# Performance work log

Hardware: AMD Instinct MI355X
Metric: run time of the kernel (lower is better)

## Reference

```python
import jax, jax.numpy as jnp
import numpy as np

B, T, C, D = 4, 2048, 48, 512
L = 16                    # transcript length per video (distinct labels)
K = 9                     # bdy_kernel
CS = 15                   # cs_kernel
N_TR = L - 1
N_CAND = 3 * N_TR         # candidate_mul * pt_num
WIN_LEN = int(T / L * 0.15)   # int(t / t_len * win_scale)
ALPHA, BETA, GAMMA, TEMP = 1.0, 1.0, 0.1, 0.1
LOG2 = float(np.log(2.0))

def _bdy_kernel():
    ker = np.zeros((K, K), np.float32)
    c = K // 2
    ker[:c, :c] = 1; ker[c:, c:] = 1
    ker[:c, c:] = -1; ker[c:, :c] = -1
    ker[c, c] = 0
    return jnp.asarray(ker)

BDY_KER = _bdy_kernel()

def bdy_score_fn(prob):
    # prob: [T, C]; sliding windows of size K over time (zero padded)
    c = K // 2
    pad = jnp.pad(prob, ((c, c), (0, 0)))
    win = pad[jnp.arange(T)[:, None] + jnp.arange(K)[None, :]]       # [T,K,C]
    p = win[:, :, None, :]                                           # [T,K,1,C]
    m = (p + win[:, None, :, :]) / 2                                 # [T,K,K,C]
    # torch F.kl_div((m+1e-32).log(), p) = p*(log p - log(m+1e-32)), xlogy(0)=0
    kl = jnp.sum(jnp.where(p > 0, p * (jnp.log(jnp.where(p > 0, p, 1.0)) - jnp.log(m + 1e-32)), 0.0), -1)
    js = (kl + jnp.swapaxes(kl, 1, 2)) / 2
    js = -(js / LOG2 * 2 - 1)                                        # [T,K,K]
    return jnp.mean(BDY_KER[None] * js, axis=(-1, -2))               # [T]

def dp(cls_score):
    # cls_score: [N_TR, N_CAND]; min-cost alignment DP, inner jj-loop vectorized
    cost = -cls_score
    n_tr, n_x = N_TR, N_CAND
    W = 2 * n_tr + 1
    col = jnp.arange(W)
    inf = jnp.float32(jnp.inf)
    tr_at = jnp.clip(col // 2, 0, n_tr - 1)
    even = (col % 2 == 0)
    ge2 = col >= 2

    def init_cols(ii):
        c0 = jnp.where(ii < n_x - n_tr, 0.0, inf)
        c1 = jnp.where(ii <= n_x - n_tr, cost[0, ii], inf)
        d1 = jnp.where(ii <= n_x - n_tr, 1, 0).astype(jnp.int32)
        return c0, c1, d1

    c0, c1, d1 = init_cols(0)
    row0 = jnp.full((W,), inf).at[0].set(c0).at[1].set(c1)
    dir0 = jnp.zeros((W,), jnp.int32).at[1].set(d1)

    def step(prev, ii):
        dm1 = jnp.concatenate([jnp.full((1,), inf), prev[:-1]])
        dm2 = jnp.concatenate([jnp.full((2,), inf), prev[:-2]])
        c_at = cost[:, ii][tr_at]
        even_val = jnp.minimum(prev, dm1)
        even_dir = jnp.where(prev < dm1, 0, 1).astype(jnp.int32)
        odd_val = c_at + jnp.minimum(dm1, dm2)
        odd_dir = jnp.where(dm1 < dm2, 1, 2).astype(jnp.int32)
        c0, c1, d1 = init_cols(ii)
        new = jnp.where(ge2, jnp.where(even, even_val, odd_val), inf)
        new = new.at[0].set(c0).at[1].set(c1)
        dirs = jnp.where(ge2, jnp.where(even, even_dir, odd_dir), 0).astype(jnp.int32)
        dirs = dirs.at[1].set(d1)
        return new, dirs

    last, dirs = jax.lax.scan(step, row0, jnp.arange(1, n_x))
    dir_mat = jnp.concatenate([dir0[None], dirs], 0)                 # [n_x, W]
    cur_j0 = jnp.where(last[2 * n_tr] < last[2 * n_tr - 1], 2 * n_tr, 2 * n_tr - 1).astype(jnp.int32)

    def bt(cur_j, x):
        ii, dir_row = x
        is_odd = (cur_j % 2) == 1
        out_idx = jnp.where(is_odd, cur_j // 2, jnp.int32(n_tr))     # n_tr = OOB -> dropped
        new_j = cur_j - dir_row[cur_j]
        return new_j, (out_idx, ii.astype(jnp.int32))

    _, (oi, ovals) = jax.lax.scan(bt, cur_j0, (jnp.arange(n_x), dir_mat), reverse=True)
    return jnp.zeros((n_tr,), jnp.int32).at[oi].set(ovals, mode='drop')

def detect(logit, tr):
    # logit: [T,C] (detached), tr: [L] ints -> boundary frame indices [N_TR]
    prob = jax.nn.softmax(logit, -1)
    score = bdy_score_fn(prob).at[0].set(-jnp.inf)
    backup = score
    pos = jnp.arange(T)

    def pick(s, _):
        i = jnp.argmax(s)
        return jnp.where(jnp.abs(pos - i) <= WIN_LEN, -jnp.inf, s), i

    _, cand = jax.lax.scan(pick, score, None, length=N_CAND)
    cand = jnp.sort(cand)                                            # [N_CAND]
    # class-transition score at candidate points
    cc = CS // 2
    pairs = jnp.pad(prob[:, tr], ((cc, cc), (0, 0)))                 # [T+2cc, L]
    win = pairs[cand[:, None] + jnp.arange(CS)[None, :]]             # [N_CAND, CS, L]
    first, second = win[:, :, :-1], win[:, :, 1:]
    k0 = jnp.where(jnp.arange(CS) < cc, 1.0, -1.0)[None, :, None]
    cls = jnp.sum(k0 * (first - second), axis=1) / (2 * CS)          # [N_CAND, N_TR]
    cls = cls.T + backup[cand][None, :]                              # [N_TR, N_CAND]
    return cand[dp(cls)]

def _forward(tok_logit, fr_logit, vid_multi_hot, feat, mask, transcript):
    y = vid_multi_hot
    tok_loss = jnp.mean(-(y * jax.nn.log_sigmoid(tok_logit) + (1 - y) * jax.nn.log_sigmoid(-tok_logit)))
    # boundary detection on detached logits
    bdy = jax.vmap(detect)(jax.lax.stop_gradient(fr_logit), transcript)   # [B, N_TR]
    pse = jax.vmap(lambda b, tr: tr[jnp.sum(jnp.arange(T)[:, None] >= b[None, :], axis=1)])(bdy, transcript)
    # frame CE (bgw==1.0 path, full mask so no -100 labels)
    logp = jax.nn.log_softmax(fr_logit, -1)
    ce = -jnp.take_along_axis(logp, pse[..., None], axis=-1)[..., 0]
    m = mask.astype(ce.dtype)
    fr_loss = jnp.sum(ce * m) / jnp.sum(m)
    # global-local contrast
    tok_feat = jax.lax.stop_gradient(feat[:, :C, :])
    fr_feat = feat[:, C:, :]

    def glc_one(tok, fr, pse_i, tr, m_i):
        labels = jnp.sort(tr)                                        # = unique(pse[mask]), distinct labels
        oh = (pse_i[None, :] == labels[:, None]).astype(fr.dtype) * m_i[None, :]
        cnt = jnp.maximum(jnp.sum(oh, 1, keepdims=True), 1.0)
        la = (oh @ fr) / cnt
        la = la / jnp.maximum(jnp.linalg.norm(la, axis=-1, keepdims=True), 1e-12)
        tk = tok / jnp.maximum(jnp.linalg.norm(tok, axis=-1, keepdims=True), 1e-12)
        sim = (la @ tk.T) / TEMP                                     # [L, C]
        return jnp.mean(-jnp.take_along_axis(jax.nn.log_softmax(sim, -1), labels[:, None], axis=-1))

    glc_loss = jnp.mean(jax.vmap(glc_one)(tok_feat, fr_feat, pse, transcript, mask.astype(feat.dtype)))
    return ALPHA * tok_loss + BETA * fr_loss + GAMMA * glc_loss

def setup_inputs() -> dict:
    key = jax.random.key(0)
    ks = jax.random.split(key, 5)
    tok_logit = jax.random.normal(ks[0], (B, C), jnp.float32)
    fr_logit = jax.random.normal(ks[1], (B, T, C), jnp.float32)
    mask = jnp.ones((B, T), bool)
    transcript = jax.vmap(lambda k: jax.random.permutation(k, C)[:L])(jax.random.split(ks[2], B)).astype(jnp.int32)
    vid_multi_hot = jax.random.uniform(ks[3], (B, C), jnp.float32)
    feat = jax.random.normal(ks[4], (B, C + T, D), jnp.float32)
    return {"epoch": 5, "tok_logit": tok_logit, "fr_logit": fr_logit, "mask": mask,
            "transcript": transcript, "vid_multi_hot": vid_multi_hot, "feat": feat}

def reference(epoch, tok_logit, fr_logit, mask, transcript, vid_multi_hot, feat):
    # epoch >= warm_epc (=0), so the full loss path runs
    return _forward(tok_logit, fr_logit, vid_multi_hot, feat, mask, transcript)
```

## Files before the change

kernel.cpp:

```cpp
#include <hip/hip_runtime.h>
#include <math.h>

#define BB 4
#define TT 2048
#define CC 48
#define DD 512
#define LL 16
#define NTR 15
#define NCAND 45
#define WINLEN 19
#define CSW 15
#define CCHALF 7

static __device__ __forceinline__ float wave_reduce_sum(float v) {
    for (int off = 32; off; off >>= 1) v += __shfl_down(v, off);
    return v;
}

#define DPPMAX(x, ctrl) fmaxf((x), __int_as_float(__builtin_amdgcn_update_dpp( \
    __float_as_int(x), __float_as_int(x), (ctrl), 0xF, 0xF, false)))

__global__ __launch_bounds__(64) void k_softmax(const float* __restrict__ fr,
                                                float* __restrict__ prob,
                                                float* __restrict__ logp,
                                                float* __restrict__ lse) {
    int row = blockIdx.x;
    int c = threadIdx.x;
    const float* x = fr + (size_t)row * CC;
    float xv = (c < CC) ? x[c] : -INFINITY;
    float m = xv;
    for (int off = 32; off; off >>= 1) m = fmaxf(m, __shfl_down(m, off));
    m = __shfl(m, 0);
    float e = (c < CC) ? expf(xv - m) : 0.f;
    float s = wave_reduce_sum(e);
    s = __shfl(s, 0);
    if (c < CC) {
        float p = e / s;
        prob[(size_t)row * CC + c] = p;
        logp[(size_t)row * CC + c] = logf(p);
    }
    if (c == 0) lse[row] = m + logf(s);
}

__global__ __launch_bounds__(64) void k_score(const float* __restrict__ prob,
                                              const float* __restrict__ logp,
                                              float* __restrict__ score) {
    int row = blockIdx.x;
    int b = row / TT, t = row % TT;
    __shared__ float sp[9][CC];
    __shared__ float slp[9][CC];
    int tid = threadIdx.x;
    for (int idx = tid; idx < 9 * CC; idx += 64) {
        int i = idx / CC, c = idx - (idx / CC) * CC;
        int r = t - 4 + i;
        float pv = 0.f, lv = 0.f;
        if (r >= 0 && r < TT) {
            pv = prob[((size_t)b * TT + r) * CC + c];
            lv = logp[((size_t)b * TT + r) * CC + c];
        }
        sp[i][c] = pv;
        slp[i][c] = lv;
    }
    __syncthreads();
    float acc = 0.f;
    for (int item = tid; item < 36 * CC; item += 64) {
        int pidx = item / CC, c = item - pidx * CC;
        int i = 0, rem = pidx;
        while (rem >= 8 - i) { rem -= 8 - i; ++i; }
        int j = i + 1 + rem;
        float wgt = ((i < 4) == (j < 4)) ? 1.f : -1.f;
        float pi = sp[i][c], pj = sp[j][c];
        float logm = logf(0.5f * (pi + pj) + 1e-32f);
        float term = 0.f;
        if (pi > 0.f) term += pi * (slp[i][c] - logm);
        if (pj > 0.f) term += pj * (slp[j][c] - logm);
        acc += wgt * term;
    }
    acc = wave_reduce_sum(acc);
    if (tid == 0) {
        const float SC = -2.0f / (81.0f * 0.6931471805599453f);
        score[row] = (t == 0) ? -INFINITY : SC * acc;
    }
}

__global__ __launch_bounds__(64) void k_pick(const float* __restrict__ score,
                                             int* __restrict__ cand) {
    int b = blockIdx.x;
    int lane = threadIdx.x;
    __shared__ float s[64 * 33];
    __shared__ int cl[NCAND];
    for (int t = lane; t < TT; t += 64) s[t + (t >> 5)] = score[(size_t)b * TT + t];
    __syncthreads();
    float v[32];
    #pragma unroll
    for (int k = 0; k < 32; ++k) v[k] = s[lane * 33 + k];
    int base = lane << 5;
    for (int it = 0; it < NCAND; ++it) {
        float best = -INFINITY; int bi = 0;
        #pragma unroll
        for (int k = 31; k >= 0; --k) {
            if (v[k] >= best) { best = v[k]; bi = k; }
        }
        float m = best;
        m = DPPMAX(m, 0x111);
        m = DPPMAX(m, 0x112);
        m = DPPMAX(m, 0x114);
        m = DPPMAX(m, 0x118);
        m = DPPMAX(m, 0x142);
        m = DPPMAX(m, 0x143);
        float gmax = __int_as_float(__builtin_amdgcn_readlane(__float_as_int(m), 63));
        unsigned long long ball = __ballot(best == gmax);
        int sl = (int)(__ffsll(ball) - 1);
        int mp = __builtin_amdgcn_readlane(base + bi, sl);
        if (lane == 0) cl[it] = mp;
        int llo = mp - WINLEN - base;
        int lhi = mp + WINLEN - base;
        unsigned lowm = (llo <= 0) ? 0xffffffffu : ((llo >= 32) ? 0u : ~((1u << llo) - 1u));
        unsigned him  = (lhi >= 31) ? 0xffffffffu : ((lhi < 0) ? 0u : ((2u << lhi) - 1u));
        unsigned wm = lowm & him;
        #pragma unroll
        for (int k = 0; k < 32; ++k)
            if (wm & (1u << k)) v[k] = -INFINITY;
    }
    __syncthreads();
    if (lane < NCAND) {
        int my = cl[lane];
        int rank = 0;
        for (int i = 0; i < NCAND; ++i) rank += (cl[i] < my) ? 1 : 0;
        cand[b * 64 + rank] = my;
    }
}

__global__ __launch_bounds__(256) void k_dp(const float* __restrict__ prob,
                                            const float* __restrict__ score,
                                            const int* __restrict__ cand,
                                            const int* __restrict__ transcript,
                                            int* __restrict__ labels_out,
                                            int* __restrict__ pse,
                                            int* __restrict__ rowmap) {
    int b = blockIdx.x;
    __shared__ float cost[NTR][NCAND];
    __shared__ int tr_s[LL];
    __shared__ int cand_s[NCAND];
    __shared__ float backup_s[NCAND];
    __shared__ signed char dir_mat[NCAND][32];
    __shared__ int bdy_s[NTR];
    __shared__ int rank_s[LL];
    int tid = threadIdx.x;
    if (tid < LL) tr_s[tid] = transcript[b * LL + tid];
    if (tid < NCAND) {
        int cp = cand[b * 64 + tid];
        cand_s[tid] = cp;
        backup_s[tid] = score[(size_t)b * TT + cp];
    }
    __syncthreads();
    for (int e = tid; e < NTR * NCAND; e += 256) {
        int j = e / NCAND, ii = e - (e / NCAND) * NCAND;
        int cpos = cand_s[ii];
        int trj = tr_s[j], trj1 = tr_s[j + 1];
        float sum = 0.f;
        for (int k = 0; k < CSW; ++k) {
            int r = cpos - CCHALF + k;
            float a = 0.f, d2 = 0.f;
            if (r >= 0 && r < TT) {
                const float* pr = prob + ((size_t)b * TT + r) * CC;
                a = pr[trj]; d2 = pr[trj1];
            }
            sum += ((k < CCHALF) ? 1.f : -1.f) * (a - d2);
        }
        cost[j][ii] = -(sum / 30.f + backup_s[ii]);
    }
    __syncthreads();
    if (tid < 64) {
        int lane = tid;
        float prev = INFINITY;
        if (lane == 0) prev = 0.f;
        if (lane == 1) prev = cost[0][0];
        if (lane < 31) dir_mat[0][lane] = (lane == 1) ? (signed char)1 : (signed char)0;
        for (int ii = 1; ii < NCAND; ++ii) {
            float dm1 = __shfl_up(prev, 1); if (lane < 1) dm1 = INFINITY;
            float dm2 = __shfl_up(prev, 2); if (lane < 2) dm2 = INFINITY;
            int trat = lane >> 1; if (trat > NTR - 1) trat = NTR - 1;
            float c_at = cost[trat][ii];
            float ev = fminf(prev, dm1);
            int ed = (prev < dm1) ? 0 : 1;
            float ov = c_at + fminf(dm1, dm2);
            int od = (dm1 < dm2) ? 1 : 2;
            float nv; int nd;
            if (lane >= 2) {
                if ((lane & 1) == 0) { nv = ev; nd = ed; }
                else { nv = ov; nd = od; }
            } else { nv = INFINITY; nd = 0; }
            if (lane == 0) { nv = (ii < NCAND - NTR) ? 0.f : INFINITY; nd = 0; }
            if (lane == 1) {
                nv = (ii <= NCAND - NTR) ? cost[0][ii] : INFINITY;
                nd = (ii <= NCAND - NTR) ? 1 : 0;
            }
            prev = nv;
            if (lane < 31) dir_mat[ii][lane] = (signed char)nd;
        }
        float v29 = __shfl(prev, 29);
        float v30 = __shfl(prev, 30);
        if (lane == 0) {
            int cur = (v30 < v29) ? 30 : 29;
            for (int ii = NCAND - 1; ii >= 0; --ii) {
                if (cur & 1) bdy_s[cur >> 1] = cand_s[ii];
                cur -= (int)dir_mat[ii][cur];
            }
            int lab[LL];
            for (int i2 = 0; i2 < LL; ++i2) lab[i2] = tr_s[i2];
            for (int a2 = 1; a2 < LL; ++a2) {
                int key = lab[a2]; int b2 = a2 - 1;
                while (b2 >= 0 && lab[b2] > key) { lab[b2 + 1] = lab[b2]; --b2; }
                lab[b2 + 1] = key;
            }
            for (int i2 = 0; i2 < LL; ++i2) labels_out[b * LL + i2] = lab[i2];
            for (int j2 = 0; j2 < LL; ++j2) {
                int r2 = 0;
                for (int l2 = 0; l2 < LL; ++l2) if (lab[l2] == tr_s[j2]) r2 = l2;
                rank_s[j2] = r2;
            }
        }
    }
    __syncthreads();
    for (int t = tid; t < TT; t += 256) {
        int cnt = 0;
        for (int j = 0; j < NTR; ++j) cnt += (t >= bdy_s[j]) ? 1 : 0;
        pse[b * TT + t] = tr_s[cnt];
        rowmap[b * TT + t] = rank_s[cnt];
    }
}

__global__ __launch_bounds__(256) void k_la(const float* __restrict__ feat,
                                            const int* __restrict__ rowmap,
                                            float* __restrict__ la) {
    int b = blockIdx.y;
    int t0 = blockIdx.x * 32;
    int tid = threadIdx.x;
    const float* fr = feat + ((size_t)b * (CC + TT) + CC) * DD;
    __shared__ int rm[32];
    if (tid < 32) rm[tid] = rowmap[b * TT + t0 + tid];
    __syncthreads();
    float ax = 0.f, ay = 0.f;
    int cur = rm[0];
    for (int k = 0; k < 32; ++k) {
        int r = rm[k];
        if (r != cur) {
            float* dst = la + ((size_t)b * LL + cur) * DD + tid * 2;
            atomicAdd(dst, ax);
            atomicAdd(dst + 1, ay);
            ax = 0.f; ay = 0.f; cur = r;
        }
        const float2* p = (const float2*)(fr + (size_t)(t0 + k) * DD);
        float2 v = p[tid];
        ax += v.x; ay += v.y;
    }
    float* dst = la + ((size_t)b * LL + cur) * DD + tid * 2;
    atomicAdd(dst, ax);
    atomicAdd(dst + 1, ay);
}

__global__ __launch_bounds__(256) void k_norms(const float* __restrict__ feat,
                                               const float* __restrict__ la,
                                               float* __restrict__ nla,
                                               float* __restrict__ ntk) {
    int wid = (blockIdx.x * 256 + threadIdx.x) >> 6;
    int lane = threadIdx.x & 63;
    const float* rowp;
    if (wid < BB * LL) rowp = la + (size_t)wid * DD;
    else {
        int k = wid - BB * LL;
        int b = k / CC, c = k - (k / CC) * CC;
        rowp = feat + ((size_t)b * (CC + TT) + c) * DD;
    }
    const float4* p = (const float4*)rowp;
    float ss = 0.f;
    for (int j = lane; j < DD / 4; j += 64) {
        float4 v = p[j];
        ss += v.x * v.x + v.y * v.y + v.z * v.z + v.w * v.w;
    }
    ss = wave_reduce_sum(ss);
    if (lane == 0) {
        float nn = fmaxf(sqrtf(ss), 1e-12f);
        if (wid < BB * LL) nla[wid] = nn; else ntk[wid - BB * LL] = nn;
    }
}

__global__ __launch_bounds__(256) void k_glc(const float* __restrict__ feat,
                                             const float* __restrict__ la,
                                             const float* __restrict__ nla,
                                             const float* __restrict__ ntk,
                                             const int* __restrict__ labels,
                                             float* __restrict__ terms) {
    int l = blockIdx.x, b = blockIdx.y;
    __shared__ float la_s[DD];
    __shared__ float sim_s[CC];
    int tid = threadIdx.x;
    const float* lar = la + ((size_t)b * LL + l) * DD;
    ((float2*)la_s)[tid] = ((const float2*)lar)[tid];
    __syncthreads();
    int wave = tid >> 6, lane = tid & 63;
    float inv_nla = 10.0f / nla[b * LL + l];
    for (int c = wave; c < CC; c += 4) {
        const float4* tr = (const float4*)(feat + ((size_t)b * (CC + TT) + c) * DD);
        const float4* ls = (const float4*)la_s;
        float dot = 0.f;
        for (int j = lane; j < DD / 4; j += 64) {
            float4 a = ls[j]; float4 v = tr[j];
            dot += a.x * v.x + a.y * v.y + a.z * v.z + a.w * v.w;
        }
        dot = wave_reduce_sum(dot);
        if (lane == 0) sim_s[c] = dot * inv_nla / ntk[b * CC + c];
    }
    __syncthreads();
    if (tid == 0) {
        float mx = -INFINITY;
        for (int c = 0; c < CC; ++c) mx = fmaxf(mx, sim_s[c]);
        float se = 0.f;
        for (int c = 0; c < CC; ++c) se += expf(sim_s[c] - mx);
        int lab = labels[b * LL + l];
        terms[b * LL + l] = (mx + logf(se)) - sim_s[lab];
    }
}

__global__ __launch_bounds__(256) void k_fr(const float* __restrict__ fr_logit,
                                            const float* __restrict__ lse,
                                            const int* __restrict__ pse,
                                            float* __restrict__ fr_acc) {
    int i = blockIdx.x * 256 + threadIdx.x;
    int p = pse[i];
    float v = lse[i] - fr_logit[(size_t)i * CC + p];
    v = wave_reduce_sum(v);
    if ((threadIdx.x & 63) == 0) atomicAdd(fr_acc, v);
}

__global__ __launch_bounds__(256) void k_combine(const float* __restrict__ tok_logit,
                                                 const float* __restrict__ vid,
                                                 const float* __restrict__ fr_acc,
                                                 const float* __restrict__ terms,
                                                 float* __restrict__ out) {
    int tid = threadIdx.x;
    __shared__ float red[4];
    float acc = 0.f;
    if (tid < BB * CC) {
        float x = tok_logit[tid], y = vid[tid];
        float lsp = fminf(x, 0.f) - log1pf(expf(-fabsf(x)));
        float lsn = fminf(-x, 0.f) - log1pf(expf(-fabsf(x)));
        acc = -(y * lsp + (1.f - y) * lsn);
    }
    float w = wave_reduce_sum(acc);
    if ((tid & 63) == 0) red[tid >> 6] = w;
    __syncthreads();
    if (tid == 0) {
        float s_tok = (red[0] + red[1] + red[2] + red[3]) / (float)(BB * CC);
        float s_fr = fr_acc[0] / (float)(BB * TT);
        float g = 0.f;
        for (int i = 0; i < BB * LL; ++i) g += terms[i];
        float glc = g / (float)(BB * LL);
        out[0] = s_tok + s_fr + 0.1f * glc;
    }
}

extern "C" void kernel_launch(void* const* d_in, const int* in_sizes, int n_in,
                              void* d_out, int out_size, void* d_ws, size_t ws_size,
                              hipStream_t stream) {
    (void)in_sizes; (void)n_in; (void)out_size; (void)ws_size;
    const float* tok_logit  = (const float*)d_in[1];
    const float* fr_logit   = (const float*)d_in[2];
    const int*   transcript = (const int*)d_in[4];
    const float* vid        = (const float*)d_in[5];
    const float* feat       = (const float*)d_in[6];

    char* ws = (char*)d_ws;
    float* prob   = (float*)(ws + 0);
    float* logp   = (float*)(ws + 1572864);
    float* lse    = (float*)(ws + 3145728);
    float* score  = (float*)(ws + 3178496);
    float* la     = (float*)(ws + 3211264);
    float* fr_acc = (float*)(ws + 3342336);
    float* terms  = (float*)(ws + 3342592);
    float* nla    = (float*)(ws + 3342848);
    float* ntk    = (float*)(ws + 3343104);
    int*   cand   = (int*)(ws + 3343872);
    int*   labels = (int*)(ws + 3344896);
    int*   pse    = (int*)(ws + 3345152);
    int*   rowmap = (int*)(ws + 3377920);
    float* out    = (float*)d_out;

    hipMemsetAsync(la, 0, 131072 + 256, stream);

    k_softmax<<<BB * TT, 64, 0, stream>>>(fr_logit, prob, logp, lse);
    k_score<<<BB * TT, 64, 0, stream>>>(prob, logp, score);
    k_pick<<<BB, 64, 0, stream>>>(score, cand);
    k_dp<<<BB, 256, 0, stream>>>(prob, score, cand, transcript, labels, pse, rowmap);
    k_la<<<dim3(TT / 32, BB), 256, 0, stream>>>(feat, rowmap, la);
    k_norms<<<64, 256, 0, stream>>>(feat, la, nla, ntk);
    k_glc<<<dim3(LL, BB), 256, 0, stream>>>(feat, la, nla, ntk, labels, terms);
    k_fr<<<BB * TT / 256, 256, 0, stream>>>(fr_logit, lse, pse, fr_acc);
    k_combine<<<1, 256, 0, stream>>>(tok_logit, vid, fr_acc, terms, out);
}
```

Measured before the change: 193.5 us.

## Fuse softmax into score, merge pick+dp, segment-based pooling, drop atomics

Replaces the softmax kernel with a per-row logsumexp kernel that packs four rows per block. Probabilities and log-probs are now recomputed on the fly from the logits in the score and DP kernels, so the prob/logp buffers are no longer written or read. The JS-divergence sum is reformulated algebraically to use one log per pair. Candidate picking and DP are merged into one kernel. Label-averaged features are pooled per contiguous segment without atomics or a memset, norms are folded into the GLC kernel, and the frame loss uses per-block partial sums. Extra exp work and fast-math intrinsics may slightly change numerics.

```diff
diff --git a/kernel.cpp b/kernel.cpp
--- a/kernel.cpp
+++ b/kernel.cpp
@@ -20,49 +20,51 @@
 #define DPPMAX(x, ctrl) fmaxf((x), __int_as_float(__builtin_amdgcn_update_dpp( \
     __float_as_int(x), __float_as_int(x), (ctrl), 0xF, 0xF, false)))
 
-__global__ __launch_bounds__(64) void k_softmax(const float* __restrict__ fr,
-                                                float* __restrict__ prob,
-                                                float* __restrict__ logp,
-                                                float* __restrict__ lse) {
-    int row = blockIdx.x;
-    int c = threadIdx.x;
-    const float* x = fr + (size_t)row * CC;
-    float xv = (c < CC) ? x[c] : -INFINITY;
+__global__ __launch_bounds__(256) void k_lse(const float* __restrict__ fr,
+                                             float* __restrict__ lse) {
+    int row = blockIdx.x * 4 + (threadIdx.x >> 6);
+    int lane = threadIdx.x & 63;
+    float xv = (lane < CC) ? fr[(size_t)row * CC + lane] : -INFINITY;
     float m = xv;
     for (int off = 32; off; off >>= 1) m = fmaxf(m, __shfl_down(m, off));
     m = __shfl(m, 0);
-    float e = (c < CC) ? expf(xv - m) : 0.f;
+    float e = (lane < CC) ? __expf(xv - m) : 0.f;
     float s = wave_reduce_sum(e);
-    s = __shfl(s, 0);
-    if (c < CC) {
-        float p = e / s;
-        prob[(size_t)row * CC + c] = p;
-        logp[(size_t)row * CC + c] = logf(p);
-    }
-    if (c == 0) lse[row] = m + logf(s);
-}
-
-__global__ __launch_bounds__(64) void k_score(const float* __restrict__ prob,
-                                              const float* __restrict__ logp,
+    if (lane == 0) lse[row] = m + __logf(s);
+}
+
+__global__ __launch_bounds__(64) void k_score(const float* __restrict__ fr,
+                                              const float* __restrict__ lse,
                                               float* __restrict__ score) {
     int row = blockIdx.x;
     int b = row / TT, t = row % TT;
     __shared__ float sp[9][CC];
     __shared__ float slp[9][CC];
-    int tid = threadIdx.x;
+    __shared__ float lse_s[9];
+    int tid = threadIdx.x;
+    if (tid < 9) {
+        int r = t - 4 + tid;
+        lse_s[tid] = (r >= 0 && r < TT) ? lse[b * TT + r] : 0.f;
+    }
+    __syncthreads();
     for (int idx = tid; idx < 9 * CC; idx += 64) {
         int i = idx / CC, c = idx - (idx / CC) * CC;
         int r = t - 4 + i;
         float pv = 0.f, lv = 0.f;
         if (r >= 0 && r < TT) {
-            pv = prob[((size_t)b * TT + r) * CC + c];
-            lv = logp[((size_t)b * TT + r) * CC + c];
+            float x = fr[((size_t)b * TT + r) * CC + c];
+            lv = x - lse_s[i];
+            pv = __expf(lv);
         }
         sp[i][c] = pv;
         slp[i][c] = lv;
     }
     __syncthreads();
     float acc = 0.f;
+    for (int idx = tid; idx < 4 * CC; idx += 64) {
+        int i = idx / CC, c = idx - (idx / CC) * CC;
+        acc += -2.f * sp[i][c] * slp[i][c];
+    }
     for (int item = tid; item < 36 * CC; item += 64) {
         int pidx = item / CC, c = item - pidx * CC;
         int i = 0, rem = pidx;
@@ -70,11 +72,8 @@
         int j = i + 1 + rem;
         float wgt = ((i < 4) == (j < 4)) ? 1.f : -1.f;
         float pi = sp[i][c], pj = sp[j][c];
-        float logm = logf(0.5f * (pi + pj) + 1e-32f);
-        float term = 0.f;
-        if (pi > 0.f) term += pi * (slp[i][c] - logm);
-        if (pj > 0.f) term += pj * (slp[j][c] - logm);
-        acc += wgt * term;
+        float logm = __logf(0.5f * (pi + pj) + 1e-32f);
+        acc -= wgt * (pi + pj) * logm;
     }
     acc = wave_reduce_sum(acc);
     if (tid == 0) {
@@ -83,62 +82,17 @@
     }
 }
 
-__global__ __launch_bounds__(64) void k_pick(const float* __restrict__ score,
-                                             int* __restrict__ cand) {
+__global__ __launch_bounds__(256) void k_pickdp(const float* __restrict__ fr,
+                                                const float* __restrict__ lse,
+                                                const float* __restrict__ score,
+                                                const int* __restrict__ transcript,
+                                                int* __restrict__ labels_out,
+                                                int* __restrict__ pse,
+                                                int* __restrict__ seg_start,
+                                                int* __restrict__ seg_end) {
     int b = blockIdx.x;
-    int lane = threadIdx.x;
     __shared__ float s[64 * 33];
     __shared__ int cl[NCAND];
-    for (int t = lane; t < TT; t += 64) s[t + (t >> 5)] = score[(size_t)b * TT + t];
-    __syncthreads();
-    float v[32];
-    #pragma unroll
-    for (int k = 0; k < 32; ++k) v[k] = s[lane * 33 + k];
-    int base = lane << 5;
-    for (int it = 0; it < NCAND; ++it) {
-        float best = -INFINITY; int bi = 0;
-        #pragma unroll
-        for (int k = 31; k >= 0; --k) {
-            if (v[k] >= best) { best = v[k]; bi = k; }
-        }
-        float m = best;
-        m = DPPMAX(m, 0x111);
-        m = DPPMAX(m, 0x112);
-        m = DPPMAX(m, 0x114);
-        m = DPPMAX(m, 0x118);
-        m = DPPMAX(m, 0x142);
-        m = DPPMAX(m, 0x143);
-        float gmax = __int_as_float(__builtin_amdgcn_readlane(__float_as_int(m), 63));
-        unsigned long long ball = __ballot(best == gmax);
-        int sl = (int)(__ffsll(ball) - 1);
-        int mp = __builtin_amdgcn_readlane(base + bi, sl);
-        if (lane == 0) cl[it] = mp;
-        int llo = mp - WINLEN - base;
-        int lhi = mp + WINLEN - base;
-        unsigned lowm = (llo <= 0) ? 0xffffffffu : ((llo >= 32) ? 0u : ~((1u << llo) - 1u));
-        unsigned him  = (lhi >= 31) ? 0xffffffffu : ((lhi < 0) ? 0u : ((2u << lhi) - 1u));
-        unsigned wm = lowm & him;
-        #pragma unroll
-        for (int k = 0; k < 32; ++k)
-            if (wm & (1u << k)) v[k] = -INFINITY;
-    }
-    __syncthreads();
-    if (lane < NCAND) {
-        int my = cl[lane];
-        int rank = 0;
-        for (int i = 0; i < NCAND; ++i) rank += (cl[i] < my) ? 1 : 0;
-        cand[b * 64 + rank] = my;
-    }
-}
-
-__global__ __launch_bounds__(256) void k_dp(const float* __restrict__ prob,
-                                            const float* __restrict__ score,
-                                            const int* __restrict__ cand,
-                                            const int* __restrict__ transcript,
-                                            int* __restrict__ labels_out,
-                                            int* __restrict__ pse,
-                                            int* __restrict__ rowmap) {
-    int b = blockIdx.x;
     __shared__ float cost[NTR][NCAND];
     __shared__ int tr_s[LL];
     __shared__ int cand_s[NCAND];
@@ -148,12 +102,52 @@
     __shared__ int rank_s[LL];
     int tid = threadIdx.x;
     if (tid < LL) tr_s[tid] = transcript[b * LL + tid];
+    for (int t = tid; t < TT; t += 256) s[t + (t >> 5)] = score[(size_t)b * TT + t];
+    __syncthreads();
+
+    if (tid < 64) {
+        int lane = tid;
+        float v[32];
+        #pragma unroll
+        for (int k = 0; k < 32; ++k) v[k] = s[lane * 33 + k];
+        int base = lane << 5;
+        for (int it = 0; it < NCAND; ++it) {
+            float best = -INFINITY; int bi = 0;
+            #pragma unroll
+            for (int k = 31; k >= 0; --k)
+                if (v[k] >= best) { best = v[k]; bi = k; }
+            float m = best;
+            m = DPPMAX(m, 0x111); m = DPPMAX(m, 0x112);
+            m = DPPMAX(m, 0x114); m = DPPMAX(m, 0x118);
+            m = DPPMAX(m, 0x142); m = DPPMAX(m, 0x143);
+            float gmax = __int_as_float(__builtin_amdgcn_readlane(__float_as_int(m), 63));
+            unsigned long long ball = __ballot(best == gmax);
+            int sl = (int)(__ffsll(ball) - 1);
+            int mp = __builtin_amdgcn_readlane(base + bi, sl);
+            if (lane == 0) cl[it] = mp;
+            int llo = mp - WINLEN - base;
+            int lhi = mp + WINLEN - base;
+            unsigned lowm = (llo <= 0) ? 0xffffffffu : ((llo >= 32) ? 0u : ~((1u << llo) - 1u));
+            unsigned him  = (lhi >= 31) ? 0xffffffffu : ((lhi < 0) ? 0u : ((2u << lhi) - 1u));
+            unsigned wm = lowm & him;
+            #pragma unroll
+            for (int k = 0; k < 32; ++k)
+                if (wm & (1u << k)) v[k] = -INFINITY;
+        }
+        if (lane < NCAND) {
+            int my = cl[lane];
+            int rank = 0;
+            for (int i = 0; i < NCAND; ++i) rank += (cl[i] < my) ? 1 : 0;
+            cand_s[rank] = my;
+        }
+    }
+    __syncthreads();
     if (tid < NCAND) {
-        int cp = cand[b * 64 + tid];
-        cand_s[tid] = cp;
-        backup_s[tid] = score[(size_t)b * TT + cp];
-    }
-    __syncthreads();
+        int cp = cand_s[tid];
+        backup_s[tid] = s[cp + (cp >> 5)];
+    }
+    __syncthreads();
+
     for (int e = tid; e < NTR * NCAND; e += 256) {
         int j = e / NCAND, ii = e - (e / NCAND) * NCAND;
         int cpos = cand_s[ii];
@@ -163,14 +157,17 @@
             int r = cpos - CCHALF + k;
             float a = 0.f, d2 = 0.f;
             if (r >= 0 && r < TT) {
-                const float* pr = prob + ((size_t)b * TT + r) * CC;
-                a = pr[trj]; d2 = pr[trj1];
+                size_t ro = (size_t)b * TT + r;
+                float ls = lse[ro];
+                a  = __expf(fr[ro * CC + trj]  - ls);
+                d2 = __expf(fr[ro * CC + trj1] - ls);
             }
             sum += ((k < CCHALF) ? 1.f : -1.f) * (a - d2);
         }
         cost[j][ii] = -(sum / 30.f + backup_s[ii]);
     }
     __syncthreads();
+
     if (tid < 64) {
         int lane = tid;
         float prev = INFINITY;
@@ -220,6 +217,12 @@
                 for (int l2 = 0; l2 < LL; ++l2) if (lab[l2] == tr_s[j2]) r2 = l2;
                 rank_s[j2] = r2;
             }
+            for (int j2 = 0; j2 < LL; ++j2) {
+                int st = (j2 == 0) ? 0 : bdy_s[j2 - 1];
+                int en = (j2 == LL - 1) ? TT : bdy_s[j2];
+                seg_start[b * LL + rank_s[j2]] = st;
+                seg_end[b * LL + rank_s[j2]] = en;
+            }
         }
     }
     __syncthreads();
@@ -227,90 +230,68 @@
         int cnt = 0;
         for (int j = 0; j < NTR; ++j) cnt += (t >= bdy_s[j]) ? 1 : 0;
         pse[b * TT + t] = tr_s[cnt];
-        rowmap[b * TT + t] = rank_s[cnt];
     }
 }
 
 __global__ __launch_bounds__(256) void k_la(const float* __restrict__ feat,
-                                            const int* __restrict__ rowmap,
+                                            const int* __restrict__ seg_start,
+                                            const int* __restrict__ seg_end,
                                             float* __restrict__ la) {
-    int b = blockIdx.y;
-    int t0 = blockIdx.x * 32;
-    int tid = threadIdx.x;
+    int l = blockIdx.x, b = blockIdx.y;
+    int st = seg_start[b * LL + l], en = seg_end[b * LL + l];
+    int wave = threadIdx.x >> 6, lane = threadIdx.x & 63;
     const float* fr = feat + ((size_t)b * (CC + TT) + CC) * DD;
-    __shared__ int rm[32];
-    if (tid < 32) rm[tid] = rowmap[b * TT + t0 + tid];
-    __syncthreads();
-    float ax = 0.f, ay = 0.f;
-    int cur = rm[0];
-    for (int k = 0; k < 32; ++k) {
-        int r = rm[k];
-        if (r != cur) {
-            float* dst = la + ((size_t)b * LL + cur) * DD + tid * 2;
-            atomicAdd(dst, ax);
-            atomicAdd(dst + 1, ay);
-            ax = 0.f; ay = 0.f; cur = r;
-        }
-        const float2* p = (const float2*)(fr + (size_t)(t0 + k) * DD);
-        float2 v = p[tid];
-        ax += v.x; ay += v.y;
-    }
-    float* dst = la + ((size_t)b * LL + cur) * DD + tid * 2;
-    atomicAdd(dst, ax);
-    atomicAdd(dst + 1, ay);
-}
-
-__global__ __launch_bounds__(256) void k_norms(const float* __restrict__ feat,
-                                               const float* __restrict__ la,
-                                               float* __restrict__ nla,
-                                               float* __restrict__ ntk) {
-    int wid = (blockIdx.x * 256 + threadIdx.x) >> 6;
-    int lane = threadIdx.x & 63;
-    const float* rowp;
-    if (wid < BB * LL) rowp = la + (size_t)wid * DD;
-    else {
-        int k = wid - BB * LL;
-        int b = k / CC, c = k - (k / CC) * CC;
-        rowp = feat + ((size_t)b * (CC + TT) + c) * DD;
-    }
-    const float4* p = (const float4*)rowp;
-    float ss = 0.f;
-    for (int j = lane; j < DD / 4; j += 64) {
-        float4 v = p[j];
-        ss += v.x * v.x + v.y * v.y + v.z * v.z + v.w * v.w;
-    }
-    ss = wave_reduce_sum(ss);
-    if (lane == 0) {
-        float nn = fmaxf(sqrtf(ss), 1e-12f);
-        if (wid < BB * LL) nla[wid] = nn; else ntk[wid - BB * LL] = nn;
-    }
+    __shared__ float part[4][DD];
+    float4 a0 = {0,0,0,0}, a1 = {0,0,0,0};
+    for (int r = st + wave; r < en; r += 4) {
+        const float4* p = (const float4*)(fr + (size_t)r * DD);
+        float4 v0 = p[lane];
+        float4 v1 = p[64 + lane];
+        a0.x += v0.x; a0.y += v0.y; a0.z += v0.z; a0.w += v0.w;
+        a1.x += v1.x; a1.y += v1.y; a1.z += v1.z; a1.w += v1.w;
+    }
+    ((float4*)part[wave])[lane] = a0;
+    ((float4*)part[wave])[64 + lane] = a1;
+    __syncthreads();
+    float* lar = la + ((size_t)b * LL + l) * DD;
+    for (int idx = threadIdx.x; idx < DD; idx += 256)
+        lar[idx] = part[0][idx] + part[1][idx] + part[2][idx] + part[3][idx];
 }
 
 __global__ __launch_bounds__(256) void k_glc(const float* __restrict__ feat,
                                              const float* __restrict__ la,
-                                             const float* __restrict__ nla,
-                                             const float* __restrict__ ntk,
                                              const int* __restrict__ labels,
                                              float* __restrict__ terms) {
     int l = blockIdx.x, b = blockIdx.y;
     __shared__ float la_s[DD];
     __shared__ float sim_s[CC];
-    int tid = threadIdx.x;
+    __shared__ float red[4];
+    __shared__ float s_inv_nla;
+    int tid = threadIdx.x;
+    int wave = tid >> 6, lane = tid & 63;
     const float* lar = la + ((size_t)b * LL + l) * DD;
-    ((float2*)la_s)[tid] = ((const float2*)lar)[tid];
-    __syncthreads();
-    int wave = tid >> 6, lane = tid & 63;
-    float inv_nla = 10.0f / nla[b * LL + l];
+    float2 lv = ((const float2*)lar)[tid];
+    ((float2*)la_s)[tid] = lv;
+    float ss = lv.x * lv.x + lv.y * lv.y;
+    ss = wave_reduce_sum(ss);
+    if (lane == 0) red[wave] = ss;
+    __syncthreads();
+    if (tid == 0)
+        s_inv_nla = 10.0f / fmaxf(sqrtf(red[0] + red[1] + red[2] + red[3]), 1e-12f);
+    __syncthreads();
     for (int c = wave; c < CC; c += 4) {
         const float4* tr = (const float4*)(feat + ((size_t)b * (CC + TT) + c) * DD);
         const float4* ls = (const float4*)la_s;
-        float dot = 0.f;
+        float dot = 0.f, vv = 0.f;
         for (int j = lane; j < DD / 4; j += 64) {
             float4 a = ls[j]; float4 v = tr[j];
             dot += a.x * v.x + a.y * v.y + a.z * v.z + a.w * v.w;
+            vv  += v.x * v.x + v.y * v.y + v.z * v.z + v.w * v.w;
         }
         dot = wave_reduce_sum(dot);
-        if (lane == 0) sim_s[c] = dot * inv_nla / ntk[b * CC + c];
+        vv  = wave_reduce_sum(vv);
+        if (lane == 0)
+            sim_s[c] = dot * s_inv_nla / fmaxf(sqrtf(vv), 1e-12f);
     }
     __syncthreads();
     if (tid == 0) {
@@ -326,17 +307,24 @@
 __global__ __launch_bounds__(256) void k_fr(const float* __restrict__ fr_logit,
                                             const float* __restrict__ lse,
                                             const int* __restrict__ pse,
-                                            float* __restrict__ fr_acc) {
-    int i = blockIdx.x * 256 + threadIdx.x;
-    int p = pse[i];
-    float v = lse[i] - fr_logit[(size_t)i * CC + p];
-    v = wave_reduce_sum(v);
-    if ((threadIdx.x & 63) == 0) atomicAdd(fr_acc, v);
+                                            float* __restrict__ fr_part) {
+    __shared__ float red[4];
+    int tid = threadIdx.x;
+    float acc = 0.f;
+    for (int k = 0; k < 4; ++k) {
+        int i = blockIdx.x * 1024 + k * 256 + tid;
+        int p = pse[i];
+        acc += lse[i] - fr_logit[(size_t)i * CC + p];
+    }
+    acc = wave_reduce_sum(acc);
+    if ((tid & 63) == 0) red[tid >> 6] = acc;
+    __syncthreads();
+    if (tid == 0) fr_part[blockIdx.x] = red[0] + red[1] + red[2] + red[3];
 }
 
 __global__ __launch_bounds__(256) void k_combine(const float* __restrict__ tok_logit,
                                                  const float* __restrict__ vid,
-                                                 const float* __restrict__ fr_acc,
+                                                 const float* __restrict__ fr_part,
                                                  const float* __restrict__ terms,
                                                  float* __restrict__ out) {
     int tid = threadIdx.x;
@@ -353,7 +341,9 @@
     __syncthreads();
     if (tid == 0) {
         float s_tok = (red[0] + red[1] + red[2] + red[3]) / (float)(BB * CC);
-        float s_fr = fr_acc[0] / (float)(BB * TT);
+        float sfr = 0.f;
+        for (int i = 0; i < 8; ++i) sfr += fr_part[i];
+        float s_fr = sfr / (float)(BB * TT);
         float g = 0.f;
         for (int i = 0; i < BB * LL; ++i) g += terms[i];
         float glc = g / (float)(BB * LL);
@@ -372,30 +362,23 @@
     const float* feat       = (const float*)d_in[6];
 
     char* ws = (char*)d_ws;
-    float* prob   = (float*)(ws + 0);
-    float* logp   = (float*)(ws + 1572864);
-    float* lse    = (float*)(ws + 3145728);
-    float* score  = (float*)(ws + 3178496);
-    float* la     = (float*)(ws + 3211264);
-    float* fr_acc = (float*)(ws + 3342336);
-    float* terms  = (float*)(ws + 3342592);
-    float* nla    = (float*)(ws + 3342848);
-    float* ntk    = (float*)(ws + 3343104);
-    int*   cand   = (int*)(ws + 3343872);
-    int*   labels = (int*)(ws + 3344896);
-    int*   pse    = (int*)(ws + 3345152);
-    int*   rowmap = (int*)(ws + 3377920);
-    float* out    = (float*)d_out;
-
-    hipMemsetAsync(la, 0, 131072 + 256, stream);
-
-    k_softmax<<<BB * TT, 64, 0, stream>>>(fr_logit, prob, logp, lse);
-    k_score<<<BB * TT, 64, 0, stream>>>(prob, logp, score);
-    k_pick<<<BB, 64, 0, stream>>>(score, cand);
-    k_dp<<<BB, 256, 0, stream>>>(prob, score, cand, transcript, labels, pse, rowmap);
-    k_la<<<dim3(TT / 32, BB), 256, 0, stream>>>(feat, rowmap, la);
-    k_norms<<<64, 256, 0, stream>>>(feat, la, nla, ntk);
-    k_glc<<<dim3(LL, BB), 256, 0, stream>>>(feat, la, nla, ntk, labels, terms);
-    k_fr<<<BB * TT / 256, 256, 0, stream>>>(fr_logit, lse, pse, fr_acc);
-    k_combine<<<1, 256, 0, stream>>>(tok_logit, vid, fr_acc, terms, out);
-}
+    float* lse     = (float*)(ws + 0);
+    float* score   = (float*)(ws + 32768);
+    float* la      = (float*)(ws + 65536);
+    float* terms   = (float*)(ws + 196608);
+    float* fr_part = (float*)(ws + 196864);
+    int*   labels  = (int*)(ws + 197120);
+    int*   pse     = (int*)(ws + 197376);
+    int*   seg_st  = (int*)(ws + 230144);
+    int*   seg_en  = (int*)(ws + 230400);
+    float* out     = (float*)d_out;
+
+    k_lse<<<BB * TT / 4, 256, 0, stream>>>(fr_logit, lse);
+    k_score<<<BB * TT, 64, 0, stream>>>(fr_logit, lse, score);
+    k_pickdp<<<BB, 256, 0, stream>>>(fr_logit, lse, score, transcript,
+                                     labels, pse, seg_st, seg_en);
+    k_fr<<<8, 256, 0, stream>>>(fr_logit, lse, pse, fr_part);
+    k_la<<<dim3(LL, BB), 256, 0, stream>>>(feat, seg_st, seg_en, la);
+    k_glc<<<dim3(LL, BB), 256, 0, stream>>>(feat, la, labels, terms);
+    k_combine<<<1, 256, 0, stream>>>(tok_logit, vid, fr_part, terms, out);
+}
```

Measured after the change: 202.9 us. 4.9% more time.
